# Performance work log

Measured on AMD Instinct MI355X. Metric: run time of the kernel, lower is better.

The kernel has to match this reference:

```python
import jax, jax.numpy as jnp
import numpy as np

# Router hyperparameters (from init_kwargs)
E = 64        # num_routed_experts
K = 6         # moe_router_topk
G = 8         # num_expert_groups
TG = 3        # topk_group
ALPHA = 0.001 # aux_loss_alpha
EPG = E // G  # experts per group


def setup_inputs() -> dict:
    key = jax.random.key(0)
    k1, k2 = jax.random.split(key)
    hidden_states = jax.random.normal(k1, (4, 4096, 4096), dtype=jnp.float32)
    # kaiming_uniform-ish scale for the gate weight [E, H]
    bound = 1.0 / np.sqrt(4096)
    weight = jax.random.uniform(k2, (E, 4096), dtype=jnp.float32,
                                minval=-bound, maxval=bound)
    return {"hidden_states": hidden_states, "weight": weight}


def reference(hidden_states, weight):
    B, S, H = hidden_states.shape
    T = B * S
    x = hidden_states.reshape(T, H).astype(jnp.float32)
    # gate GEMM + softmax scoring
    logits = jnp.einsum('th,eh->te', x, weight.astype(jnp.float32))  # [T, E]
    scores = jax.nn.softmax(logits, axis=-1)
    # group-limited greedy: keep only experts in the top-TG groups (by group max)
    group_scores = scores.reshape(T, G, EPG).max(axis=-1)            # [T, G]
    _, group_idx = jax.lax.top_k(group_scores, TG)                   # [T, TG]
    group_mask = jnp.zeros((T, G), scores.dtype).at[
        jnp.arange(T)[:, None], group_idx].set(1.0)                  # [T, G]
    score_mask = jnp.repeat(group_mask, EPG, axis=-1)                # [T, E]
    tmp_scores = jnp.where(score_mask > 0, scores, 0.0)
    topk_weight, topk_idx = jax.lax.top_k(tmp_scores, K)             # [T, K]
    # norm_topk_prob = True and top_k > 1 -> normalize
    topk_weight = topk_weight / (topk_weight.sum(axis=-1, keepdims=True) + 1e-20)
    # sequence-level aux loss (seq_aux=True, training, alpha > 0)
    idx_aux = topk_idx.reshape(B, S * K)                             # [B, S*K]
    ce = jax.vmap(lambda idx: jnp.zeros(E, jnp.float32).at[idx].add(1.0))(idx_aux)
    ce = ce / (S * K / E)                                            # [B, E]
    aux_loss = (ce * scores.reshape(B, S, E).mean(axis=1)).sum(axis=1).mean() * ALPHA
    return topk_idx, topk_weight, aux_loss
```

## Files before the change

kernel.cpp:

```cpp
#include <hip/hip_runtime.h>
#include <math.h>

#define TTOK   16384
#define HDIM   4096
#define ENUM   64
#define KTOP   6
#define GNUM   8
#define TGK    3
#define BBATCH 4
#define SSEQ   4096
#define ALPHAC 0.001f

#define KSPLIT 2
#define BM     64
#define BK     64
#define KH     (HDIM / KSPLIT)
#define NIT    (KH / BK)
#define XSTR   68
#define WSTR   68

__global__ __launch_bounds__(256, 2)
void gate_gemm(const float* __restrict__ X, const float* __restrict__ W,
               float* __restrict__ lp) {
    __shared__ __align__(16) float Xs[BM * XSTR];
    __shared__ __align__(16) float Ws[BK * WSTR];

    const int tid  = threadIdx.x;
    const int bid  = blockIdx.x;
    const int tile = bid & 255;
    const int half = bid >> 8;
    const int tok0 = tile * BM;
    const int k0   = half * KH;

    const int tx = tid & 15;
    const int ty = tid >> 4;

    const int c4  = tid & 15;
    const int rw  = tid >> 4;

    float acc[4][4];
#pragma unroll
    for (int r = 0; r < 4; ++r)
#pragma unroll
        for (int c = 0; c < 4; ++c) acc[r][c] = 0.f;

    float4 xst[4], wst[4];

#pragma unroll
    for (int p = 0; p < 4; ++p) {
        const int row = p * 16 + rw;
        xst[p] = *(const float4*)(X + (size_t)(tok0 + row) * HDIM + k0 + c4 * 4);
        wst[p] = *(const float4*)(W + (size_t)row * HDIM + k0 + c4 * 4);
    }

    for (int it = 0; it < NIT; ++it) {
        __syncthreads();
#pragma unroll
        for (int p = 0; p < 4; ++p) {
            const int row = p * 16 + rw;
            *(float4*)(Xs + row * XSTR + c4 * 4) = xst[p];
            Ws[(c4 * 4 + 0) * WSTR + row] = wst[p].x;
            Ws[(c4 * 4 + 1) * WSTR + row] = wst[p].y;
            Ws[(c4 * 4 + 2) * WSTR + row] = wst[p].z;
            Ws[(c4 * 4 + 3) * WSTR + row] = wst[p].w;
        }
        __syncthreads();

        if (it + 1 < NIT) {
            const int kk = k0 + (it + 1) * BK;
#pragma unroll
            for (int p = 0; p < 4; ++p) {
                const int row = p * 16 + rw;
                xst[p] = *(const float4*)(X + (size_t)(tok0 + row) * HDIM + kk + c4 * 4);
                wst[p] = *(const float4*)(W + (size_t)row * HDIM + kk + c4 * 4);
            }
        }

#pragma unroll
        for (int ks = 0; ks < BK; ks += 4) {
            float4 xv[4], wv[4];
#pragma unroll
            for (int r = 0; r < 4; ++r)
                xv[r] = *(const float4*)(Xs + (4 * ty + r) * XSTR + ks);
#pragma unroll
            for (int j = 0; j < 4; ++j)
                wv[j] = *(const float4*)(Ws + (ks + j) * WSTR + 4 * tx);
#pragma unroll
            for (int r = 0; r < 4; ++r) {
                const float* xf = (const float*)&xv[r];
#pragma unroll
                for (int j = 0; j < 4; ++j) {
                    const float* wf = (const float*)&wv[j];
#pragma unroll
                    for (int c = 0; c < 4; ++c)
                        acc[r][c] = fmaf(xf[j], wf[c], acc[r][c]);
                }
            }
        }
    }

#pragma unroll
    for (int r = 0; r < 4; ++r) {
        float4 v = make_float4(acc[r][0], acc[r][1], acc[r][2], acc[r][3]);
        *(float4*)(lp + (size_t)half * TTOK * ENUM
                      + (size_t)(tok0 + 4 * ty + r) * ENUM + 4 * tx) = v;
    }
}

__global__ __launch_bounds__(256)
void router_topk(const float* __restrict__ lp,
                 float* __restrict__ out_idx, float* __restrict__ out_w,
                 float* __restrict__ ssum_g, int* __restrict__ cnt_g) {
    __shared__ float s_ssum[ENUM];
    __shared__ int   s_cnt[ENUM];
    const int tid = threadIdx.x;
    if (tid < ENUM) { s_ssum[tid] = 0.f; s_cnt[tid] = 0; }
    __syncthreads();

    const int lane = tid & 63;
    const int wv   = tid >> 6;
    const int g    = lane >> 3;

    float ss_local = 0.f;
    int   cnt_local = 0;

    const int tok_base = blockIdx.x * 64 + wv * 16;

    for (int i = 0; i < 16; ++i) {
        const int t = tok_base + i;
        float logit = lp[(size_t)t * ENUM + lane]
                    + lp[(size_t)TTOK * ENUM + (size_t)t * ENUM + lane];

        float m = logit;
#pragma unroll
        for (int off = 32; off; off >>= 1) m = fmaxf(m, __shfl_xor(m, off));
        float ex = expf(logit - m);
        float sum = ex;
#pragma unroll
        for (int off = 32; off; off >>= 1) sum += __shfl_xor(sum, off);
        const float score = ex / sum;

        float gm = score;
#pragma unroll
        for (int off = 1; off < 8; off <<= 1) gm = fmaxf(gm, __shfl_xor(gm, off));

        int rank = 0;
#pragma unroll
        for (int gg = 0; gg < GNUM; ++gg) {
            float gvo = __shfl(gm, gg * 8);
            rank += (gvo > gm) || (gvo == gm && gg < g);
        }
        const bool sel_group = (rank < TGK);
        const float ms = sel_group ? score : 0.0f;

        int   taken = 0;
        float my_i = 0.f, my_w = 0.f;
        float wsum = 0.f;
#pragma unroll
        for (int j = 0; j < KTOP; ++j) {
            float v = taken ? -1.0f : ms;
            int   idx = lane;
#pragma unroll
            for (int off = 32; off; off >>= 1) {
                float vo = __shfl_xor(v, off);
                int   io = __shfl_xor(idx, off);
                if (vo > v || (vo == v && io < idx)) { v = vo; idx = io; }
            }
            wsum += v;
            if (lane == idx) taken = 1;
            if (lane == j) { my_i = (float)idx; my_w = v; }
        }
        const float inv = 1.0f / (wsum + 1e-20f);
        if (lane < KTOP) {
            out_idx[(size_t)t * KTOP + lane] = my_i;
            out_w[(size_t)t * KTOP + lane]   = my_w * inv;
        }

        ss_local += score;
        cnt_local += taken;
    }

    atomicAdd(&s_ssum[lane], ss_local);
    atomicAdd(&s_cnt[lane], cnt_local);
    __syncthreads();

    const int b = (blockIdx.x * 64) / SSEQ;
    if (tid < ENUM) {
        atomicAdd(&ssum_g[b * ENUM + tid], s_ssum[tid]);
        atomicAdd(&cnt_g[b * ENUM + tid], s_cnt[tid]);
    }
}

__global__ __launch_bounds__(256)
void aux_loss(const float* __restrict__ ssum_g, const int* __restrict__ cnt_g,
              float* __restrict__ out_aux) {
    const int tid = threadIdx.x;
    float v = (float)cnt_g[tid] * (float)ENUM / ((float)SSEQ * (float)KTOP)
            * (ssum_g[tid] / (float)SSEQ);
#pragma unroll
    for (int off = 32; off; off >>= 1) v += __shfl_xor(v, off);
    __shared__ float red[4];
    if ((tid & 63) == 0) red[tid >> 6] = v;
    __syncthreads();
    if (tid == 0)
        out_aux[0] = (red[0] + red[1] + red[2] + red[3]) * (ALPHAC / (float)BBATCH);
}

extern "C" void kernel_launch(void* const* d_in, const int* in_sizes, int n_in,
                              void* d_out, int out_size, void* d_ws, size_t ws_size,
                              hipStream_t stream) {
    const float* X = (const float*)d_in[0];
    const float* W = (const float*)d_in[1];

    float* out     = (float*)d_out;
    float* out_idx = out;
    float* out_w   = out + (size_t)TTOK * KTOP;
    float* out_aux = out + (size_t)2 * TTOK * KTOP;

    float* lp     = (float*)d_ws;
    float* ssum_g = lp + (size_t)KSPLIT * TTOK * ENUM;
    int*   cnt_g  = (int*)(ssum_g + BBATCH * ENUM);

    hipMemsetAsync(ssum_g, 0, BBATCH * ENUM * (sizeof(float) + sizeof(int)), stream);

    gate_gemm<<<256 * KSPLIT, 256, 0, stream>>>(X, W, lp);
    router_topk<<<TTOK / 64, 256, 0, stream>>>(lp, out_idx, out_w, ssum_g, cnt_g);
    aux_loss<<<1, 256, 0, stream>>>(ssum_g, cnt_g, out_aux);
}
```

Baseline: 509.6 us.

## Pre-transpose gate weight, raise split-K to four, serialize router per token

After: 573.3 us. +12.5%, slower.

```diff
diff --git a/kernel.cpp b/kernel.cpp
--- a/kernel.cpp
+++ b/kernel.cpp
@@ -11,7 +11,7 @@
 #define SSEQ   4096
 #define ALPHAC 0.001f
 
-#define KSPLIT 2
+#define KSPLIT 4
 #define BM     64
 #define BK     64
 #define KH     (HDIM / KSPLIT)
@@ -19,8 +19,36 @@
 #define XSTR   68
 #define WSTR   68
 
-__global__ __launch_bounds__(256, 2)
-void gate_gemm(const float* __restrict__ X, const float* __restrict__ W,
+__global__ __launch_bounds__(256)
+void transpose_w(const float* __restrict__ W, float* __restrict__ Wt) {
+    __shared__ float T[64 * 65];
+    const int tid = threadIdx.x;
+    const int k0  = blockIdx.x * 64;
+#pragma unroll
+    for (int r = 0; r < 4; ++r) {
+        const int q = r * 256 + tid;
+        const int e = q >> 4, c4 = q & 15;
+        float4 v = *(const float4*)(W + (size_t)e * HDIM + k0 + c4 * 4);
+        float* d = T + e * 65 + c4 * 4;
+        d[0] = v.x; d[1] = v.y; d[2] = v.z; d[3] = v.w;
+    }
+    __syncthreads();
+#pragma unroll
+    for (int r = 0; r < 4; ++r) {
+        const int q  = r * 256 + tid;
+        const int k  = q >> 4;
+        const int e4 = (q & 15) * 4;
+        float4 v;
+        v.x = T[(e4 + 0) * 65 + k];
+        v.y = T[(e4 + 1) * 65 + k];
+        v.z = T[(e4 + 2) * 65 + k];
+        v.w = T[(e4 + 3) * 65 + k];
+        *(float4*)(Wt + (size_t)(k0 + k) * ENUM + e4) = v;
+    }
+}
+
+__global__ __launch_bounds__(256, 4)
+void gate_gemm(const float* __restrict__ X, const float* __restrict__ Wt,
                float* __restrict__ lp) {
     __shared__ __align__(16) float Xs[BM * XSTR];
     __shared__ __align__(16) float Ws[BK * WSTR];
@@ -35,8 +63,8 @@
     const int tx = tid & 15;
     const int ty = tid >> 4;
 
-    const int c4  = tid & 15;
-    const int rw  = tid >> 4;
+    const int c4 = tid & 15;
+    const int rw = tid >> 4;
 
     float acc[4][4];
 #pragma unroll
@@ -50,7 +78,7 @@
     for (int p = 0; p < 4; ++p) {
         const int row = p * 16 + rw;
         xst[p] = *(const float4*)(X + (size_t)(tok0 + row) * HDIM + k0 + c4 * 4);
-        wst[p] = *(const float4*)(W + (size_t)row * HDIM + k0 + c4 * 4);
+        wst[p] = *(const float4*)(Wt + (size_t)(k0 + row) * ENUM + c4 * 4);
     }
 
     for (int it = 0; it < NIT; ++it) {
@@ -59,10 +87,7 @@
         for (int p = 0; p < 4; ++p) {
             const int row = p * 16 + rw;
             *(float4*)(Xs + row * XSTR + c4 * 4) = xst[p];
-            Ws[(c4 * 4 + 0) * WSTR + row] = wst[p].x;
-            Ws[(c4 * 4 + 1) * WSTR + row] = wst[p].y;
-            Ws[(c4 * 4 + 2) * WSTR + row] = wst[p].z;
-            Ws[(c4 * 4 + 3) * WSTR + row] = wst[p].w;
+            *(float4*)(Ws + row * WSTR + c4 * 4) = wst[p];
         }
         __syncthreads();
 
@@ -72,7 +97,7 @@
             for (int p = 0; p < 4; ++p) {
                 const int row = p * 16 + rw;
                 xst[p] = *(const float4*)(X + (size_t)(tok0 + row) * HDIM + kk + c4 * 4);
-                wst[p] = *(const float4*)(W + (size_t)row * HDIM + kk + c4 * 4);
+                wst[p] = *(const float4*)(Wt + (size_t)(kk + row) * ENUM + c4 * 4);
             }
         }
 
@@ -107,84 +132,107 @@
     }
 }
 
+#define RTOK 64
 __global__ __launch_bounds__(256)
 void router_topk(const float* __restrict__ lp,
                  float* __restrict__ out_idx, float* __restrict__ out_w,
                  float* __restrict__ ssum_g, int* __restrict__ cnt_g) {
+    __shared__ float Ls[RTOK * 67];
+    __shared__ float s_m[RTOK], s_inv[RTOK];
     __shared__ float s_ssum[ENUM];
     __shared__ int   s_cnt[ENUM];
+
     const int tid = threadIdx.x;
-    if (tid < ENUM) { s_ssum[tid] = 0.f; s_cnt[tid] = 0; }
-    __syncthreads();
-
-    const int lane = tid & 63;
-    const int wv   = tid >> 6;
-    const int g    = lane >> 3;
-
-    float ss_local = 0.f;
-    int   cnt_local = 0;
-
-    const int tok_base = blockIdx.x * 64 + wv * 16;
-
-    for (int i = 0; i < 16; ++i) {
-        const int t = tok_base + i;
-        float logit = lp[(size_t)t * ENUM + lane]
-                    + lp[(size_t)TTOK * ENUM + (size_t)t * ENUM + lane];
-
-        float m = logit;
-#pragma unroll
-        for (int off = 32; off; off >>= 1) m = fmaxf(m, __shfl_xor(m, off));
-        float ex = expf(logit - m);
-        float sum = ex;
-#pragma unroll
-        for (int off = 32; off; off >>= 1) sum += __shfl_xor(sum, off);
-        const float score = ex / sum;
-
-        float gm = score;
-#pragma unroll
-        for (int off = 1; off < 8; off <<= 1) gm = fmaxf(gm, __shfl_xor(gm, off));
-
-        int rank = 0;
-#pragma unroll
-        for (int gg = 0; gg < GNUM; ++gg) {
-            float gvo = __shfl(gm, gg * 8);
-            rank += (gvo > gm) || (gvo == gm && gg < g);
-        }
-        const bool sel_group = (rank < TGK);
-        const float ms = sel_group ? score : 0.0f;
-
-        int   taken = 0;
-        float my_i = 0.f, my_w = 0.f;
-        float wsum = 0.f;
-#pragma unroll
-        for (int j = 0; j < KTOP; ++j) {
-            float v = taken ? -1.0f : ms;
-            int   idx = lane;
-#pragma unroll
-            for (int off = 32; off; off >>= 1) {
-                float vo = __shfl_xor(v, off);
-                int   io = __shfl_xor(idx, off);
-                if (vo > v || (vo == v && io < idx)) { v = vo; idx = io; }
-            }
-            wsum += v;
-            if (lane == idx) taken = 1;
-            if (lane == j) { my_i = (float)idx; my_w = v; }
-        }
-        const float inv = 1.0f / (wsum + 1e-20f);
-        if (lane < KTOP) {
-            out_idx[(size_t)t * KTOP + lane] = my_i;
-            out_w[(size_t)t * KTOP + lane]   = my_w * inv;
-        }
-
-        ss_local += score;
-        cnt_local += taken;
-    }
-
-    atomicAdd(&s_ssum[lane], ss_local);
-    atomicAdd(&s_cnt[lane], cnt_local);
-    __syncthreads();
-
-    const int b = (blockIdx.x * 64) / SSEQ;
+    const int t0  = blockIdx.x * RTOK;
+    if (tid < ENUM) { s_cnt[tid] = 0; s_ssum[tid] = 0.f; }
+
+#pragma unroll
+    for (int r = 0; r < 4; ++r) {
+        const int q  = r * 256 + tid;
+        const int t  = q >> 4, c4 = q & 15;
+        const size_t base = (size_t)(t0 + t) * ENUM + c4 * 4;
+        float4 v = *(const float4*)(lp + base);
+#pragma unroll
+        for (int h = 1; h < KSPLIT; ++h) {
+            float4 u = *(const float4*)(lp + (size_t)h * TTOK * ENUM + base);
+            v.x += u.x; v.y += u.y; v.z += u.z; v.w += u.w;
+        }
+        float* d = Ls + t * 67 + c4 * 4;
+        d[0] = v.x; d[1] = v.y; d[2] = v.z; d[3] = v.w;
+    }
+    __syncthreads();
+
+    if (tid < RTOK) {
+        const float* row = Ls + tid * 67;
+
+        float gm[GNUM];
+#pragma unroll
+        for (int g = 0; g < GNUM; ++g) {
+            float mg = row[g * 8];
+#pragma unroll
+            for (int j = 1; j < 8; ++j) mg = fmaxf(mg, row[g * 8 + j]);
+            gm[g] = mg;
+        }
+        float m = gm[0];
+#pragma unroll
+        for (int g = 1; g < GNUM; ++g) m = fmaxf(m, gm[g]);
+
+        int selmask = 0;
+#pragma unroll
+        for (int g = 0; g < GNUM; ++g) {
+            int rank = 0;
+#pragma unroll
+            for (int g2 = 0; g2 < GNUM; ++g2)
+                rank += (gm[g2] > gm[g]) || (gm[g2] == gm[g] && g2 < g);
+            selmask |= (rank < TGK) << g;
+        }
+
+        float v0=-1.f,v1=-1.f,v2=-1.f,v3=-1.f,v4=-1.f,v5=-1.f;
+        float i0=0.f,i1=0.f,i2=0.f,i3=0.f,i4=0.f,i5=0.f;
+        float s = 0.f;
+#pragma unroll
+        for (int e = 0; e < ENUM; ++e) {
+            const float ex = expf(row[e] - m);
+            s += ex;
+            const float cand = ((selmask >> (e >> 3)) & 1) ? ex : -1.0f;
+            const float fe = (float)e;
+            const bool b0 = cand > v0, b1 = cand > v1, b2 = cand > v2,
+                       b3 = cand > v3, b4 = cand > v4, b5 = cand > v5;
+            v5 = b4 ? v4 : (b5 ? cand : v5);  i5 = b4 ? i4 : (b5 ? fe : i5);
+            v4 = b3 ? v3 : (b4 ? cand : v4);  i4 = b3 ? i3 : (b4 ? fe : i4);
+            v3 = b2 ? v2 : (b3 ? cand : v3);  i3 = b2 ? i2 : (b3 ? fe : i3);
+            v2 = b1 ? v1 : (b2 ? cand : v2);  i2 = b1 ? i1 : (b2 ? fe : i2);
+            v1 = b0 ? v0 : (b1 ? cand : v1);  i1 = b0 ? i0 : (b1 ? fe : i1);
+            v0 = b0 ? cand : v0;              i0 = b0 ? fe : i0;
+        }
+        const float invw = 1.0f / (v0 + v1 + v2 + v3 + v4 + v5);
+        const int t = t0 + tid;
+        float* oi = out_idx + (size_t)t * KTOP;
+        float* ow = out_w   + (size_t)t * KTOP;
+        oi[0]=i0; oi[1]=i1; oi[2]=i2; oi[3]=i3; oi[4]=i4; oi[5]=i5;
+        ow[0]=v0*invw; ow[1]=v1*invw; ow[2]=v2*invw;
+        ow[3]=v3*invw; ow[4]=v4*invw; ow[5]=v5*invw;
+
+        atomicAdd(&s_cnt[(int)i0], 1); atomicAdd(&s_cnt[(int)i1], 1);
+        atomicAdd(&s_cnt[(int)i2], 1); atomicAdd(&s_cnt[(int)i3], 1);
+        atomicAdd(&s_cnt[(int)i4], 1); atomicAdd(&s_cnt[(int)i5], 1);
+        s_m[tid] = m; s_inv[tid] = 1.0f / s;
+    }
+    __syncthreads();
+
+    {
+        const int e = tid & 63, strip = tid >> 6;
+        float acc = 0.f;
+#pragma unroll
+        for (int i = 0; i < RTOK / 4; ++i) {
+            const int t = strip * (RTOK / 4) + i;
+            acc += expf(Ls[t * 67 + e] - s_m[t]) * s_inv[t];
+        }
+        atomicAdd(&s_ssum[e], acc);
+    }
+    __syncthreads();
+
+    const int b = t0 / SSEQ;
     if (tid < ENUM) {
         atomicAdd(&ssum_g[b * ENUM + tid], s_ssum[tid]);
         atomicAdd(&cnt_g[b * ENUM + tid], s_cnt[tid]);
@@ -218,12 +266,14 @@
     float* out_aux = out + (size_t)2 * TTOK * KTOP;
 
     float* lp     = (float*)d_ws;
-    float* ssum_g = lp + (size_t)KSPLIT * TTOK * ENUM;
+    float* Wt     = lp + (size_t)KSPLIT * TTOK * ENUM;
+    float* ssum_g = Wt + (size_t)HDIM * ENUM;
     int*   cnt_g  = (int*)(ssum_g + BBATCH * ENUM);
 
     hipMemsetAsync(ssum_g, 0, BBATCH * ENUM * (sizeof(float) + sizeof(int)), stream);
 
-    gate_gemm<<<256 * KSPLIT, 256, 0, stream>>>(X, W, lp);
-    router_topk<<<TTOK / 64, 256, 0, stream>>>(lp, out_idx, out_w, ssum_g, cnt_g);
+    transpose_w<<<HDIM / 64, 256, 0, stream>>>(W, Wt);
+    gate_gemm<<<256 * KSPLIT, 256, 0, stream>>>(X, Wt, lp);
+    router_topk<<<TTOK / RTOK, 256, 0, stream>>>(lp, out_idx, out_w, ssum_g, cnt_g);
     aux_loss<<<1, 256, 0, stream>>>(ssum_g, cnt_g, out_aux);
 }
```
